# Kernel tuning notes

Hardware: AMD Instinct MI355X
Metric: run time of the kernel (lower is better)

The kernel has to match this reference:

```python
import jax, jax.numpy as jnp
import numpy as np

SUB_NO = 20
T_NO = 200
NB = 19            # cos_basis_no
COS_SHIFT = 1.0
COS_SCALE = 5.0
T_DATA = 100000
E_NO = 2000
I_NO = 400


def _cos_basis():
    x = jnp.arange(T_NO, dtype=jnp.float32)
    raw = COS_SCALE * jnp.log(x + COS_SHIFT)                      # [T_no]
    phi = (jnp.pi / 2.0) * jnp.arange(NB, dtype=jnp.float32)[:, None]  # [NB,1]
    basis = 0.5 * jnp.cos(raw[None, :] - phi) + 0.5               # [NB, T_no]
    mask = (raw[None, :] >= phi - jnp.pi) & (raw[None, :] <= phi + jnp.pi)
    return jnp.where(mask, basis, 0.0)


def _gconv(x, kern_flipped):
    # depthwise (grouped) 1d cross-correlation, VALID padding, matching torch F.conv1d
    # x: [L, sub], kern_flipped: [sub, T_no] (already time-flipped) -> [L - T_no + 1, sub]
    out = jax.lax.conv_general_dilated(
        x.T[None],                      # [1, sub, L]
        kern_flipped[:, None, :],       # [sub, 1, T_no]
        window_strides=(1,), padding='VALID',
        feature_group_count=x.shape[1],
        dimension_numbers=('NCH', 'OIH', 'NCH'))
    return out[0].T


def setup_inputs() -> dict:
    key = jax.random.key(0)
    ks = jax.random.split(key, 16)
    rng = np.random.default_rng(0)
    # tree adjacency: each node j>0 has a parent < j; C_den[parent, child] = 1
    C_den = np.zeros((SUB_NO, SUB_NO), np.float32)
    for j in range(1, SUB_NO):
        C_den[rng.integers(0, j), j] = 1.0
    # one-hot synapse -> subunit maps
    C_syn_e = np.zeros((SUB_NO, E_NO), np.float32)
    C_syn_e[rng.integers(0, SUB_NO, E_NO), np.arange(E_NO)] = 1.0
    C_syn_i = np.zeros((SUB_NO, I_NO), np.float32)
    C_syn_i[rng.integers(0, SUB_NO, I_NO), np.arange(I_NO)] = 1.0
    # sparse binary spike trains
    S_e = (jax.random.uniform(ks[0], (T_DATA, E_NO)) < 0.02).astype(jnp.float32)
    S_i = (jax.random.uniform(ks[1], (T_DATA, I_NO)) < 0.02).astype(jnp.float32)
    Z = (jax.random.uniform(ks[2], (T_DATA, SUB_NO)) < 0.05).astype(jnp.float32)
    return {
        'S_e': S_e, 'S_i': S_i, 'Z': Z,
        'C_den': jnp.asarray(C_den), 'C_syn_e': jnp.asarray(C_syn_e), 'C_syn_i': jnp.asarray(C_syn_i),
        'W_syn': 0.1 * jax.random.normal(ks[3], (SUB_NO, NB, 2)),
        'W_hist': 0.1 * jax.random.normal(ks[4], (SUB_NO, NB)),
        'W_spk': jnp.ones(SUB_NO) + 0.05 * jax.random.normal(ks[5], (SUB_NO,)),
        'Delta_spk': jax.random.uniform(ks[6], (SUB_NO,), maxval=2.0),
        'Tau_spk': 3.0 * jnp.ones(SUB_NO) + 0.1 * jax.random.normal(ks[7], (SUB_NO,)),
        'V_o': jax.random.normal(ks[8], (1,)),
        'Theta': 0.1 * jax.random.normal(ks[9], (SUB_NO,)),
        'weight1': 0.1 * jax.random.normal(ks[10], (SUB_NO, 6)),
        'weight2': 0.1 * jax.random.normal(ks[11], (6, 6)),
        'weight3': 0.1 * jax.random.normal(ks[12], (6, SUB_NO)),
    }


def reference(S_e, S_i, Z, C_den, C_syn_e, C_syn_i, W_syn, W_hist, W_spk,
              Delta_spk, Tau_spk, V_o, Theta, weight1, weight2, weight3):
    cb = _cos_basis()                                  # [NB, T_no]
    sub = C_den.shape[0]
    pad = lambda x, n: jnp.concatenate([jnp.zeros((n, sub), x.dtype), x], axis=0)

    # --- spike_convolve ---
    syn_e = S_e @ C_syn_e.T                            # [T, sub]
    syn_i = S_i @ C_syn_i.T
    e_kern = W_syn[:, :, 0] @ cb                       # [sub, T_no]
    i_kern = W_syn[:, :, 1] @ cb
    filtered_e = _gconv(pad(syn_e, T_NO - 1), jnp.flip(e_kern, 1))
    filtered_i = _gconv(pad(syn_i, T_NO - 1), jnp.flip(i_kern, 1))
    syn = filtered_e + filtered_i                      # [T, sub]

    # --- history and spike kernels (causal, 1-step delayed: pad T_no, drop last) ---
    hist_kern = W_hist @ cb                            # [sub, T_no]
    pad_Z = pad(Z, T_NO)                               # [T + T_no, sub]
    hist_filt = _gconv(pad_Z, jnp.flip(hist_kern, 1))[:-1]   # [T, sub]

    t = jnp.maximum(jnp.arange(T_NO, dtype=jnp.float32)[None, :] - Delta_spk[:, None], 0.0)
    t_tau = t / (Tau_spk[:, None] ** 2)
    spk_kern = t_tau * jnp.exp(-t_tau) * (W_spk[:, None] ** 2)  # [sub, T_no]
    spk_filt = _gconv(pad_Z, jnp.flip(spk_kern, 1))[:-1]        # [T, sub]

    # --- per-subunit loop, vectorized: leaf gather == spk_filt @ C_den.T ---
    sub_in = syn + Theta[None, :] + hist_filt + spk_filt @ C_den.T   # [T, sub]
    h0 = jax.nn.leaky_relu(sub_in)
    h1 = jax.nn.leaky_relu(h0[:, :, None] * weight1[None, :, :])     # [T, sub, 6]
    h2 = jax.nn.leaky_relu(jnp.einsum('tsk,kj->tsj', h1, weight2))   # [T, sub, 6]
    final_Z = jax.nn.sigmoid(jnp.einsum('tsj,js->ts', h2, weight3))  # [T, sub]

    final_V = spk_filt[:, 0] + V_o[0]                  # [T]
    out_filters = jnp.concatenate([e_kern, i_kern, hist_kern, spk_kern], axis=0)  # [4*sub, T_no]
    return final_V, final_Z, out_filters
```

## Files before the change

kernel.cpp:

```cpp
#include <hip/hip_runtime.h>

typedef unsigned short ushort_t;
typedef unsigned int uint_t;
typedef float __attribute__((ext_vector_type(4))) f32x4;

#define T_DATA 100000
#define E_NO 2000
#define I_NO 400
#define SUB 20
#define TNO 200
#define NBASIS 19
#define HEAD 256
#define TAILPAD 2048
#define SIGSTRIDE (HEAD + T_DATA + TAILPAD)
#define TILE 2048
#define RPT 8
#define TSPAN 32
#define ACCSTR 36

#define OFF_Z  ((size_t)T_DATA)
#define OFF_F  ((size_t)T_DATA + (size_t)T_DATA*SUB)

__device__ __forceinline__ float b2f(ushort_t u) {
    union { uint_t i; float f; } v; v.i = ((uint_t)u) << 16; return v.f;
}
__device__ __forceinline__ ushort_t f2b(float f) {
    union { uint_t i; float f_; } v; v.f_ = f;
    uint_t b = v.i;
    uint_t r = (b + 0x7FFFu + ((b >> 16) & 1u)) >> 16;
    return (ushort_t)r;
}
__device__ __forceinline__ float ldin(const void* p, size_t idx, int mode) {
    return mode ? b2f(((const ushort_t*)p)[idx]) : ((const float*)p)[idx];
}
__device__ __forceinline__ void stout(void* p, size_t idx, float val, int mode) {
    if (mode) ((ushort_t*)p)[idx] = f2b(val);
    else      ((float*)p)[idx] = val;
}
__device__ __forceinline__ float f4get(const float4& v, int i) {
    return i == 0 ? v.x : i == 1 ? v.y : i == 2 ? v.z : v.w;
}
__device__ __forceinline__ float pick12(const float4& L, const float4& M, const float4& H, int e) {
    return e < 4 ? f4get(L, e) : e < 8 ? f4get(M, e - 4) : f4get(H, e - 8);
}
__device__ __forceinline__ int detect_mode(const void* tau) {
    const ushort_t* tu = (const ushort_t*)tau;
    int cnt = 0;
    #pragma unroll
    for (int i = 0; i < 20; ++i) {
        float v = b2f(tu[i]);
        if (v >= 1.5f && v < 6.0f) cnt++;
    }
    return (cnt >= 15) ? 1 : 0;
}

__global__ __launch_bounds__(256) void k0_prep(
        const void* Csyn_e, const void* Csyn_i,
        const void* W_syn, const void* W_hist,
        const void* W_spk, const void* Delta, const void* Tau,
        float* ws_f, int* mape, int* mapi, ushort_t* sigs, void* dout) {
    __shared__ int smode;
    int bid = blockIdx.x, tid = threadIdx.x;
    if (tid == 0) smode = detect_mode(Tau);
    __syncthreads();
    int mode = smode;
    if (bid < 80) {
        int kidx = bid / 20, s = bid % 20;
        int tau = tid;
        if (tau < TNO) {
            float val;
            if (kidx < 3) {
                float raw = 5.0f * logf((float)tau + 1.0f);
                val = 0.f;
                for (int b = 0; b < NBASIS; ++b) {
                    float phi = 1.5707963267948966f * (float)b;
                    float d = raw - phi;
                    float basis = (d >= -3.14159265358979f && d <= 3.14159265358979f)
                                  ? (0.5f * cosf(d) + 0.5f) : 0.f;
                    float w = (kidx == 0) ? ldin(W_syn, (size_t)s * NBASIS * 2 + b * 2 + 0, mode)
                            : (kidx == 1) ? ldin(W_syn, (size_t)s * NBASIS * 2 + b * 2 + 1, mode)
                                          : ldin(W_hist, (size_t)s * NBASIS + b, mode);
                    val += w * basis;
                }
            } else {
                float dl = ldin(Delta, s, mode), tu = ldin(Tau, s, mode), wk = ldin(W_spk, s, mode);
                float t = fmaxf((float)tau - dl, 0.f);
                float tt = t / (tu * tu);
                val = tt * expf(-tt) * (wk * wk);
            }
            ws_f[kidx * 4000 + s * TNO + tau] = val;
            stout(dout, OFF_F + (size_t)bid * TNO + tau, val, mode);
        }
    } else if (bid < 96) {
        int e = (bid - 80) * 256 + tid;
        if (e < E_NO) {
            int m = 0;
            for (int s = 0; s < SUB; ++s)
                if (ldin(Csyn_e, (size_t)s * E_NO + e, mode) != 0.f) { m = s; break; }
            mape[e] = m;
        }
    } else if (bid < 98) {
        int e = (bid - 96) * 256 + tid;
        if (e < I_NO) {
            int m = 0;
            for (int s = 0; s < SUB; ++s)
                if (ldin(Csyn_i, (size_t)s * I_NO + e, mode) != 0.f) { m = s; break; }
            mapi[e] = m;
        }
    } else if (bid < 158) {
        int rg = bid - 98;
        int sg = rg / 20, s = rg % 20;
        ushort_t* p = sigs + (size_t)sg * SUB * SIGSTRIDE + (size_t)s * SIGSTRIDE;
        for (int i = tid; i < HEAD; i += 256) p[i] = 0;
        for (int i = tid; i < TAILPAD; i += 256) p[HEAD + T_DATA + i] = 0;
    }
}

__global__ __launch_bounds__(256, 4) void k1_reduce(
        const void* __restrict__ S_e, const void* __restrict__ S_i,
        const void* __restrict__ Z,
        const int* __restrict__ mape, const int* __restrict__ mapi,
        const void* __restrict__ Tau,
        ushort_t* __restrict__ sigs) {
    __shared__ float acc[60 * ACCSTR];
    __shared__ int smode;
    int tid = threadIdx.x;
    if (tid == 0) smode = detect_mode(Tau);
    for (int i = tid; i < 60 * ACCSTR; i += 256) acc[i] = 0.f;
    __syncthreads();
    int mode = smode;

    int be[8], bi8[8];
    if (mode) {
        if (tid < 250) {
            #pragma unroll
            for (int j = 0; j < 8; ++j) be[j] = mape[tid * 8 + j] * ACCSTR;
        }
        if (tid < 50) {
            #pragma unroll
            for (int j = 0; j < 8; ++j) bi8[j] = (20 + mapi[tid * 8 + j]) * ACCSTR;
        }
    } else {
        if (tid < 250) {
            #pragma unroll
            for (int j = 0; j < 4; ++j) be[j] = mape[tid * 4 + j] * ACCSTR;
            #pragma unroll
            for (int j = 0; j < 4; ++j) be[4 + j] = mape[(tid + 250) * 4 + j] * ACCSTR;
        }
        if (tid < 100) {
            #pragma unroll
            for (int j = 0; j < 4; ++j) bi8[j] = (20 + mapi[tid * 4 + j]) * ACCSTR;
        }
    }

    int base = blockIdx.x * TSPAN;
    if (mode) {
        for (int r0 = 0; r0 < TSPAN; r0 += 4) {
            uint4 u[4];
            uint4 w[4];
            float zv[4];
            if (tid < 250) {
                #pragma unroll
                for (int k = 0; k < 4; ++k)
                    u[k] = *(const uint4*)((const ushort_t*)S_e +
                                           (size_t)(base + r0 + k) * E_NO + tid * 8);
            }
            if (tid < 50) {
                #pragma unroll
                for (int k = 0; k < 4; ++k)
                    w[k] = *(const uint4*)((const ushort_t*)S_i +
                                           (size_t)(base + r0 + k) * I_NO + tid * 8);
            }
            if (tid >= 192 && tid < 212) {
                int s = tid - 192;
                #pragma unroll
                for (int k = 0; k < 4; ++k)
                    zv[k] = b2f(((const ushort_t*)Z)[(size_t)(base + r0 + k) * SUB + s]);
            }
            if (tid < 250) {
                #pragma unroll
                for (int k = 0; k < 4; ++k) {
                    int rl = r0 + k;
                    uint_t wd[4] = {u[k].x, u[k].y, u[k].z, u[k].w};
                    #pragma unroll
                    for (int q = 0; q < 4; ++q) {
                        float a = b2f((ushort_t)(wd[q] & 0xFFFF));
                        float b = b2f((ushort_t)(wd[q] >> 16));
                        if (a != 0.f) atomicAdd(&acc[be[2 * q] + rl], a);
                        if (b != 0.f) atomicAdd(&acc[be[2 * q + 1] + rl], b);
                    }
                }
            }
            if (tid < 50) {
                #pragma unroll
                for (int k = 0; k < 4; ++k) {
                    int rl = r0 + k;
                    uint_t wd[4] = {w[k].x, w[k].y, w[k].z, w[k].w};
                    #pragma unroll
                    for (int q = 0; q < 4; ++q) {
                        float a = b2f((ushort_t)(wd[q] & 0xFFFF));
                        float b = b2f((ushort_t)(wd[q] >> 16));
                        if (a != 0.f) atomicAdd(&acc[bi8[2 * q] + rl], a);
                        if (b != 0.f) atomicAdd(&acc[bi8[2 * q + 1] + rl], b);
                    }
                }
            }
            if (tid >= 192 && tid < 212) {
                int s = tid - 192;
                #pragma unroll
                for (int k = 0; k < 4; ++k)
                    acc[(40 + s) * ACCSTR + r0 + k] = zv[k];
            }
        }
    } else {
        f32x4 uA[8], uB[8];
        f32x4 wv[4];
        float zv[4];
        const float* Sef = (const float*)S_e;
        const float* Sif = (const float*)S_i;
        const float* Zf  = (const float*)Z;
        bool le = (tid < 250);
        bool li = (tid < 100);
        bool lz = (tid >= 192 && tid < 212);
        if (le) {
            #pragma unroll
            for (int k = 0; k < 4; ++k) {
                const float* pe = Sef + (size_t)(base + k) * E_NO;
                uA[2 * k]     = __builtin_nontemporal_load((const f32x4*)(pe + tid * 4));
                uA[2 * k + 1] = __builtin_nontemporal_load((const f32x4*)(pe + (tid + 250) * 4));
            }
        }
        for (int r0 = 0; r0 < TSPAN; r0 += 8) {
            if (le) {
                #pragma unroll
                for (int k = 0; k < 4; ++k) {
                    const float* pe = Sef + (size_t)(base + r0 + 4 + k) * E_NO;
                    uB[2 * k]     = __builtin_nontemporal_load((const f32x4*)(pe + tid * 4));
                    uB[2 * k + 1] = __builtin_nontemporal_load((const f32x4*)(pe + (tid + 250) * 4));
                }
            }
            if (li) {
                #pragma unroll
                for (int k = 0; k < 4; ++k)
                    wv[k] = __builtin_nontemporal_load(
                        (const f32x4*)(Sif + (size_t)(base + r0 + k) * I_NO + tid * 4));
            }
            if (lz) {
                int s = tid - 192;
                #pragma unroll
                for (int k = 0; k < 4; ++k)
                    zv[k] = Zf[(size_t)(base + r0 + k) * SUB + s];
            }
            if (le) {
                #pragma unroll
                for (int k = 0; k < 4; ++k) {
                    int rl = r0 + k;
                    #pragma unroll
                    for (int q = 0; q < 4; ++q) {
                        float a = uA[2 * k][q];
                        float b = uA[2 * k + 1][q];
                        if (a != 0.f) atomicAdd(&acc[be[q] + rl], a);
                        if (b != 0.f) atomicAdd(&acc[be[4 + q] + rl], b);
                    }
                }
            }
            if (li) {
                #pragma unroll
                for (int k = 0; k < 4; ++k) {
                    int rl = r0 + k;
                    #pragma unroll
                    for (int q = 0; q < 4; ++q) {
                        float c = wv[k][q];
                        if (c != 0.f) atomicAdd(&acc[bi8[q] + rl], c);
                    }
                }
            }
            if (lz) {
                int s = tid - 192;
                #pragma unroll
                for (int k = 0; k < 4; ++k)
                    acc[(40 + s) * ACCSTR + r0 + k] = zv[k];
            }
            if (r0 + 8 < TSPAN && le) {
                #pragma unroll
                for (int k = 0; k < 4; ++k) {
                    const float* pe = Sef + (size_t)(base + r0 + 8 + k) * E_NO;
                    uA[2 * k]     = __builtin_nontemporal_load((const f32x4*)(pe + tid * 4));
                    uA[2 * k + 1] = __builtin_nontemporal_load((const f32x4*)(pe + (tid + 250) * 4));
                }
            }
            if (li) {
                #pragma unroll
                for (int k = 0; k < 4; ++k)
                    wv[k] = __builtin_nontemporal_load(
                        (const f32x4*)(Sif + (size_t)(base + r0 + 4 + k) * I_NO + tid * 4));
            }
            if (lz) {
                int s = tid - 192;
                #pragma unroll
                for (int k = 0; k < 4; ++k)
                    zv[k] = Zf[(size_t)(base + r0 + 4 + k) * SUB + s];
            }
            if (le) {
                #pragma unroll
                for (int k = 0; k < 4; ++k) {
                    int rl = r0 + 4 + k;
                    #pragma unroll
                    for (int q = 0; q < 4; ++q) {
                        float a = uB[2 * k][q];
                        float b = uB[2 * k + 1][q];
                        if (a != 0.f) atomicAdd(&acc[be[q] + rl], a);
                        if (b != 0.f) atomicAdd(&acc[be[4 + q] + rl], b);
                    }
                }
            }
            if (li) {
                #pragma unroll
                for (int k = 0; k < 4; ++k) {
                    int rl = r0 + 4 + k;
                    #pragma unroll
                    for (int q = 0; q < 4; ++q) {
                        float c = wv[k][q];
                        if (c != 0.f) atomicAdd(&acc[bi8[q] + rl], c);
                    }
                }
            }
            if (lz) {
                int s = tid - 192;
                #pragma unroll
                for (int k = 0; k < 4; ++k)
                    acc[(40 + s) * ACCSTR + r0 + 4 + k] = zv[k];
            }
        }
    }
    __syncthreads();

    for (int idx = tid; idx < 60 * (TSPAN / 4); idx += 256) {
        int sig = idx >> 3;
        int g = idx & 7;
        int t0 = g * 4;
        const float* src = &acc[sig * ACCSTR + t0];
        float4 v = *(const float4*)src;
        uint2 o;
        o.x = (uint_t)f2b(v.x) | ((uint_t)f2b(v.y) << 16);
        o.y = (uint_t)f2b(v.z) | ((uint_t)f2b(v.w) << 16);
        *(uint2*)(sigs + (size_t)sig * SIGSTRIDE + HEAD + base + t0) = o;
    }
}

__global__ __launch_bounds__(256) void k2_conv(
        const ushort_t* __restrict__ sigs, const float* __restrict__ ws_f,
        ushort_t* __restrict__ base_out, ushort_t* __restrict__ spk_out) {
    __shared__ float X[3 * 2248 + 800];
    float* XE = X;
    float* XI = X + 2248;
    float* ZZ = X + 4496;
    float* KK = X + 6744;
    int s = blockIdx.y;
    int t0 = blockIdx.x * TILE;
    int tid = threadIdx.x;

    for (int k = 0; k < 4; ++k)
        for (int j = tid; j < TNO; j += 256)
            KK[k * TNO + j] = ws_f[k * 4000 + s * TNO + j];

    {
        const ushort_t* g0 = sigs + (size_t)s * SIGSTRIDE + (HEAD - 200) + t0;
        const ushort_t* g1 = g0 + (size_t)SUB * SIGSTRIDE;
        const ushort_t* g2 = g0 + (size_t)2 * SUB * SIGSTRIDE;
        for (int v = tid; v < 281; v += 256) {
            uint4 u = *(const uint4*)(g0 + v * 8);
            float* d = XE + v * 8;
            d[0]=b2f((ushort_t)(u.x&0xFFFF)); d[1]=b2f((ushort_t)(u.x>>16));
            d[2]=b2f((ushort_t)(u.y&0xFFFF)); d[3]=b2f((ushort_t)(u.y>>16));
            d[4]=b2f((ushort_t)(u.z&0xFFFF)); d[5]=b2f((ushort_t)(u.z>>16));
            d[6]=b2f((ushort_t)(u.w&0xFFFF)); d[7]=b2f((ushort_t)(u.w>>16));
        }
        for (int v = tid; v < 281; v += 256) {
            uint4 u = *(const uint4*)(g1 + v * 8);
            float* d = XI + v * 8;
            d[0]=b2f((ushort_t)(u.x&0xFFFF)); d[1]=b2f((ushort_t)(u.x>>16));
            d[2]=b2f((ushort_t)(u.y&0xFFFF)); d[3]=b2f((ushort_t)(u.y>>16));
            d[4]=b2f((ushort_t)(u.z&0xFFFF)); d[5]=b2f((ushort_t)(u.z>>16));
            d[6]=b2f((ushort_t)(u.w&0xFFFF)); d[7]=b2f((ushort_t)(u.w>>16));
        }
        for (int v = tid; v < 281; v += 256) {
            uint4 u = *(const uint4*)(g2 + v * 8);
            float* d = ZZ + v * 8;
            d[0]=b2f((ushort_t)(u.x&0xFFFF)); d[1]=b2f((ushort_t)(u.x>>16));
            d[2]=b2f((ushort_t)(u.y&0xFFFF)); d[3]=b2f((ushort_t)(u.y>>16));
            d[4]=b2f((ushort_t)(u.z&0xFFFF)); d[5]=b2f((ushort_t)(u.z>>16));
            d[6]=b2f((ushort_t)(u.w&0xFFFF)); d[7]=b2f((ushort_t)(u.w>>16));
        }
    }
    __syncthreads();

    float acc[RPT] = {0,0,0,0,0,0,0,0};
    float spk[RPT] = {0,0,0,0,0,0,0,0};
    const float4* XE4 = (const float4*)XE;
    const float4* XI4 = (const float4*)XI;
    const float4* ZZ4 = (const float4*)ZZ;
    const float4* KE4 = (const float4*)(KK);
    const float4* KI4 = (const float4*)(KK + 200);
    const float4* KH4 = (const float4*)(KK + 400);
    const float4* KS4 = (const float4*)(KK + 600);
    int w4 = 2 * tid + 49;
    float4 eL = XE4[w4], eM = XE4[w4 + 1], eH = XE4[w4 + 2];
    float4 iL = XI4[w4], iM = XI4[w4 + 1], iH = XI4[w4 + 2];
    float4 zL = ZZ4[w4], zM = ZZ4[w4 + 1], zH = ZZ4[w4 + 2];

    for (int c = 0; c < 50; ++c) {
        if (c > 0) {
            eH = eM; eM = eL; eL = XE4[w4 - c];
            iH = iM; iM = iL; iL = XI4[w4 - c];
            zH = zM; zM = zL; zL = ZZ4[w4 - c];
        }
        float4 ke = KE4[c], ki = KI4[c], kh = KH4[c], ks = KS4[c];
        #pragma unroll
        for (int u = 0; u < 4; ++u) {
            float keu = f4get(ke, u), kiu = f4get(ki, u);
            float khu = f4get(kh, u), ksu = f4get(ks, u);
            #pragma unroll
            for (int r = 0; r < RPT; ++r) {
                float xe = pick12(eL, eM, eH, 4 + r - u);
                float xi = pick12(iL, iM, iH, 4 + r - u);
                float zz = pick12(zL, zM, zH, 3 + r - u);
                acc[r] += keu * xe;
                acc[r] += kiu * xi;
                acc[r] += khu * zz;
                spk[r] += ksu * zz;
            }
        }
    }
    int tbase = t0 + RPT * tid;
    if (tbase + RPT <= T_DATA) {
        uint4 pb, pq;
        pb.x = (uint_t)f2b(acc[0]) | ((uint_t)f2b(acc[1]) << 16);
        pb.y = (uint_t)f2b(acc[2]) | ((uint_t)f2b(acc[3]) << 16);
        pb.z = (uint_t)f2b(acc[4]) | ((uint_t)f2b(acc[5]) << 16);
        pb.w = (uint_t)f2b(acc[6]) | ((uint_t)f2b(acc[7]) << 16);
        pq.x = (uint_t)f2b(spk[0]) | ((uint_t)f2b(spk[1]) << 16);
        pq.y = (uint_t)f2b(spk[2]) | ((uint_t)f2b(spk[3]) << 16);
        pq.z = (uint_t)f2b(spk[4]) | ((uint_t)f2b(spk[5]) << 16);
        pq.w = (uint_t)f2b(spk[6]) | ((uint_t)f2b(spk[7]) << 16);
        *(uint4*)(base_out + (size_t)s * T_DATA + tbase) = pb;
        *(uint4*)(spk_out + (size_t)s * T_DATA + tbase) = pq;
    } else {
        #pragma unroll
        for (int r = 0; r < RPT; ++r) {
            int t = tbase + r;
            if (t < T_DATA) {
                base_out[(size_t)s * T_DATA + t] = f2b(acc[r]);
                spk_out[(size_t)s * T_DATA + t] = f2b(spk[r]);
            }
        }
    }
}

__global__ __launch_bounds__(256) void k3_mlp(
        const ushort_t* __restrict__ base_out, const ushort_t* __restrict__ spk_out,
        const void* __restrict__ C_den, const void* __restrict__ Theta,
        const void* __restrict__ Vo,
        const void* __restrict__ w1, const void* __restrict__ w2,
        const void* __restrict__ w3,
        const void* __restrict__ Tau,
        void* __restrict__ dout) {
    __shared__ float cd[400], th[20], W1[120], W2[36], W3[120];
    __shared__ float vo;
    __shared__ int smode;
    int tid = threadIdx.x;
    if (tid == 0) smode = detect_mode(Tau);
    __syncthreads();
    int mode = smode;
    for (int i = tid; i < 400; i += 256) cd[i] = ldin(C_den, i, mode);
    if (tid < 20) th[tid] = ldin(Theta, tid, mode);
    if (tid < 120) W1[tid] = ldin(w1, tid, mode);
    if (tid < 36) W2[tid] = ldin(w2, tid, mode);
    if (tid >= 128 && tid < 248) W3[tid - 128] = ldin(w3, tid - 128, mode);
    if (tid == 0) vo = ldin(Vo, 0, mode);
    __syncthreads();
    int t = blockIdx.x * 256 + tid;
    if (t >= T_DATA) return;
    float sv[20], bv[20];
    #pragma unroll
    for (int c = 0; c < 20; ++c) {
        sv[c] = b2f(spk_out[(size_t)c * T_DATA + t]);
        bv[c] = b2f(base_out[(size_t)c * T_DATA + t]);
    }
    stout(dout, (size_t)t, sv[0] + vo, mode);
    #pragma unroll
    for (int p = 0; p < 20; ++p) {
        float ps = 0.f;
        #pragma unroll
        for (int c = 0; c < 20; ++c) ps += cd[p * 20 + c] * sv[c];
        float x = bv[p] + th[p] + ps;
        float h0 = x >= 0.f ? x : 0.01f * x;
        float h1[6];
        #pragma unroll
        for (int k = 0; k < 6; ++k) {
            float y = h0 * W1[p * 6 + k];
            h1[k] = y >= 0.f ? y : 0.01f * y;
        }
        float zacc = 0.f;
        #pragma unroll
        for (int j = 0; j < 6; ++j) {
            float a = 0.f;
            #pragma unroll
            for (int k = 0; k < 6; ++k) a += h1[k] * W2[k * 6 + j];
            float h2 = a >= 0.f ? a : 0.01f * a;
            zacc += h2 * W3[j * 20 + p];
        }
        float zv = 1.f / (1.f + expf(-zacc));
        stout(dout, OFF_Z + (size_t)t * SUB + p, zv, mode);
    }
}

extern "C" void kernel_launch(void* const* d_in, const int* in_sizes, int n_in,
                              void* d_out, int out_size, void* d_ws, size_t ws_size,
                              hipStream_t stream) {
    const void* S_e     = d_in[0];
    const void* S_i     = d_in[1];
    const void* Z       = d_in[2];
    const void* C_den   = d_in[3];
    const void* C_syn_e = d_in[4];
    const void* C_syn_i = d_in[5];
    const void* W_syn   = d_in[6];
    const void* W_hist  = d_in[7];
    const void* W_spk   = d_in[8];
    const void* Delta   = d_in[9];
    const void* Tau     = d_in[10];
    const void* Vo      = d_in[11];
    const void* Theta   = d_in[12];
    const void* w1      = d_in[13];
    const void* w2      = d_in[14];
    const void* w3      = d_in[15];

    char* w = (char*)d_ws;
    float*    ws_f     = (float*)(w + 64);
    int*      mape     = (int*)(w + 64 + 64000);
    int*      mapi     = (int*)(w + 64 + 64000 + 8000);
    ushort_t* sigs     = (ushort_t*)(w + 73664);
    ushort_t* base_out = (ushort_t*)(w + 12350144);
    ushort_t* spk_out  = (ushort_t*)(w + 16350144);

    hipLaunchKernelGGL(k0_prep, dim3(158), dim3(256), 0, stream,
                       C_syn_e, C_syn_i, W_syn, W_hist, W_spk, Delta, Tau,
                       ws_f, mape, mapi, sigs, d_out);
    hipLaunchKernelGGL(k1_reduce, dim3(T_DATA / TSPAN), dim3(256), 0, stream,
                       S_e, S_i, Z, mape, mapi, Tau, sigs);
    hipLaunchKernelGGL(k2_conv, dim3((T_DATA + TILE - 1) / TILE, SUB), dim3(256), 0, stream,
                       sigs, ws_f, base_out, spk_out);
    hipLaunchKernelGGL(k3_mlp, dim3((T_DATA + 255) / 256), dim3(256), 0, stream,
                       base_out, spk_out, C_den, Theta, Vo, w1, w2, w3, Tau, d_out);
}
```

Measured before the change: 270.3 us.

## Double conv outputs per thread and tile size; use cached loads in reduce

The conv kernel now computes 16 outputs per thread over a 4096-sample tile instead of 8 over 2048. Each loaded input and kernel value is reused across more accumulators, and the shared memory buffers and tail padding grow to match. Separately, the reduce kernel switches from nontemporal loads to ordinary loads for the spike trains. The larger tile raises register and LDS use, which could lower occupancy, and it halves the block count along time.

```diff
diff --git a/kernel.cpp b/kernel.cpp
--- a/kernel.cpp
+++ b/kernel.cpp
@@ -11,10 +11,10 @@
 #define TNO 200
 #define NBASIS 19
 #define HEAD 256
-#define TAILPAD 2048
+#define TAILPAD 2560
 #define SIGSTRIDE (HEAD + T_DATA + TAILPAD)
-#define TILE 2048
-#define RPT 8
+#define TILE 4096
+#define RPT 16
 #define TSPAN 32
 #define ACCSTR 36
 
@@ -40,8 +40,11 @@
 __device__ __forceinline__ float f4get(const float4& v, int i) {
     return i == 0 ? v.x : i == 1 ? v.y : i == 2 ? v.z : v.w;
 }
-__device__ __forceinline__ float pick12(const float4& L, const float4& M, const float4& H, int e) {
-    return e < 4 ? f4get(L, e) : e < 8 ? f4get(M, e - 4) : f4get(H, e - 8);
+__device__ __forceinline__ float pick20(const float4& a, const float4& b, const float4& c,
+                                        const float4& d, const float4& e, int i) {
+    return i < 8 ? (i < 4 ? f4get(a, i) : f4get(b, i - 4))
+                 : (i < 12 ? f4get(c, i - 8)
+                           : (i < 16 ? f4get(d, i - 12) : f4get(e, i - 16)));
 }
 __device__ __forceinline__ int detect_mode(const void* tau) {
     const ushort_t* tu = (const ushort_t*)tau;
@@ -226,8 +229,8 @@
             #pragma unroll
             for (int k = 0; k < 4; ++k) {
                 const float* pe = Sef + (size_t)(base + k) * E_NO;
-                uA[2 * k]     = __builtin_nontemporal_load((const f32x4*)(pe + tid * 4));
-                uA[2 * k + 1] = __builtin_nontemporal_load((const f32x4*)(pe + (tid + 250) * 4));
+                uA[2 * k]     = *(const f32x4*)(pe + tid * 4);
+                uA[2 * k + 1] = *(const f32x4*)(pe + (tid + 250) * 4);
             }
         }
         for (int r0 = 0; r0 < TSPAN; r0 += 8) {
@@ -235,15 +238,14 @@
                 #pragma unroll
                 for (int k = 0; k < 4; ++k) {
                     const float* pe = Sef + (size_t)(base + r0 + 4 + k) * E_NO;
-                    uB[2 * k]     = __builtin_nontemporal_load((const f32x4*)(pe + tid * 4));
-                    uB[2 * k + 1] = __builtin_nontemporal_load((const f32x4*)(pe + (tid + 250) * 4));
+                    uB[2 * k]     = *(const f32x4*)(pe + tid * 4);
+                    uB[2 * k + 1] = *(const f32x4*)(pe + (tid + 250) * 4);
                 }
             }
             if (li) {
                 #pragma unroll
                 for (int k = 0; k < 4; ++k)
-                    wv[k] = __builtin_nontemporal_load(
-                        (const f32x4*)(Sif + (size_t)(base + r0 + k) * I_NO + tid * 4));
+                    wv[k] = *(const f32x4*)(Sif + (size_t)(base + r0 + k) * I_NO + tid * 4);
             }
             if (lz) {
                 int s = tid - 192;
@@ -285,15 +287,14 @@
                 #pragma unroll
                 for (int k = 0; k < 4; ++k) {
                     const float* pe = Sef + (size_t)(base + r0 + 8 + k) * E_NO;
-                    uA[2 * k]     = __builtin_nontemporal_load((const f32x4*)(pe + tid * 4));
-                    uA[2 * k + 1] = __builtin_nontemporal_load((const f32x4*)(pe + (tid + 250) * 4));
+                    uA[2 * k]     = *(const f32x4*)(pe + tid * 4);
+                    uA[2 * k + 1] = *(const f32x4*)(pe + (tid + 250) * 4);
                 }
             }
             if (li) {
                 #pragma unroll
                 for (int k = 0; k < 4; ++k)
-                    wv[k] = __builtin_nontemporal_load(
-                        (const f32x4*)(Sif + (size_t)(base + r0 + 4 + k) * I_NO + tid * 4));
+                    wv[k] = *(const f32x4*)(Sif + (size_t)(base + r0 + 4 + k) * I_NO + tid * 4);
             }
             if (lz) {
                 int s = tid - 192;
@@ -351,11 +352,11 @@
 __global__ __launch_bounds__(256) void k2_conv(
         const ushort_t* __restrict__ sigs, const float* __restrict__ ws_f,
         ushort_t* __restrict__ base_out, ushort_t* __restrict__ spk_out) {
-    __shared__ float X[3 * 2248 + 800];
+    __shared__ float X[3 * 4296 + 800];
     float* XE = X;
-    float* XI = X + 2248;
-    float* ZZ = X + 4496;
-    float* KK = X + 6744;
+    float* XI = X + 4296;
+    float* ZZ = X + 8592;
+    float* KK = X + 12888;
     int s = blockIdx.y;
     int t0 = blockIdx.x * TILE;
     int tid = threadIdx.x;
@@ -368,7 +369,7 @@
         const ushort_t* g0 = sigs + (size_t)s * SIGSTRIDE + (HEAD - 200) + t0;
         const ushort_t* g1 = g0 + (size_t)SUB * SIGSTRIDE;
         const ushort_t* g2 = g0 + (size_t)2 * SUB * SIGSTRIDE;
-        for (int v = tid; v < 281; v += 256) {
+        for (int v = tid; v < 537; v += 256) {
             uint4 u = *(const uint4*)(g0 + v * 8);
             float* d = XE + v * 8;
             d[0]=b2f((ushort_t)(u.x&0xFFFF)); d[1]=b2f((ushort_t)(u.x>>16));
@@ -376,7 +377,7 @@
             d[4]=b2f((ushort_t)(u.z&0xFFFF)); d[5]=b2f((ushort_t)(u.z>>16));
             d[6]=b2f((ushort_t)(u.w&0xFFFF)); d[7]=b2f((ushort_t)(u.w>>16));
         }
-        for (int v = tid; v < 281; v += 256) {
+        for (int v = tid; v < 537; v += 256) {
             uint4 u = *(const uint4*)(g1 + v * 8);
             float* d = XI + v * 8;
             d[0]=b2f((ushort_t)(u.x&0xFFFF)); d[1]=b2f((ushort_t)(u.x>>16));
@@ -384,7 +385,7 @@
             d[4]=b2f((ushort_t)(u.z&0xFFFF)); d[5]=b2f((ushort_t)(u.z>>16));
             d[6]=b2f((ushort_t)(u.w&0xFFFF)); d[7]=b2f((ushort_t)(u.w>>16));
         }
-        for (int v = tid; v < 281; v += 256) {
+        for (int v = tid; v < 537; v += 256) {
             uint4 u = *(const uint4*)(g2 + v * 8);
             float* d = ZZ + v * 8;
             d[0]=b2f((ushort_t)(u.x&0xFFFF)); d[1]=b2f((ushort_t)(u.x>>16));
@@ -395,8 +396,9 @@
     }
     __syncthreads();
 
-    float acc[RPT] = {0,0,0,0,0,0,0,0};
-    float spk[RPT] = {0,0,0,0,0,0,0,0};
+    float acc[RPT], spk[RPT];
+    #pragma unroll
+    for (int r = 0; r < RPT; ++r) { acc[r] = 0.f; spk[r] = 0.f; }
     const float4* XE4 = (const float4*)XE;
     const float4* XI4 = (const float4*)XI;
     const float4* ZZ4 = (const float4*)ZZ;
@@ -404,16 +406,16 @@
     const float4* KI4 = (const float4*)(KK + 200);
     const float4* KH4 = (const float4*)(KK + 400);
     const float4* KS4 = (const float4*)(KK + 600);
-    int w4 = 2 * tid + 49;
-    float4 eL = XE4[w4], eM = XE4[w4 + 1], eH = XE4[w4 + 2];
-    float4 iL = XI4[w4], iM = XI4[w4 + 1], iH = XI4[w4 + 2];
-    float4 zL = ZZ4[w4], zM = ZZ4[w4 + 1], zH = ZZ4[w4 + 2];
+    int w4 = 4 * tid + 49;
+    float4 e0 = XE4[w4], e1 = XE4[w4+1], e2 = XE4[w4+2], e3 = XE4[w4+3], e4 = XE4[w4+4];
+    float4 i0 = XI4[w4], i1 = XI4[w4+1], i2 = XI4[w4+2], i3 = XI4[w4+3], i4 = XI4[w4+4];
+    float4 z0 = ZZ4[w4], z1 = ZZ4[w4+1], z2 = ZZ4[w4+2], z3 = ZZ4[w4+3], z4 = ZZ4[w4+4];
 
     for (int c = 0; c < 50; ++c) {
         if (c > 0) {
-            eH = eM; eM = eL; eL = XE4[w4 - c];
-            iH = iM; iM = iL; iL = XI4[w4 - c];
-            zH = zM; zM = zL; zL = ZZ4[w4 - c];
+            e4 = e3; e3 = e2; e2 = e1; e1 = e0; e0 = XE4[w4 - c];
+            i4 = i3; i3 = i2; i2 = i1; i1 = i0; i0 = XI4[w4 - c];
+            z4 = z3; z3 = z2; z2 = z1; z1 = z0; z0 = ZZ4[w4 - c];
         }
         float4 ke = KE4[c], ki = KI4[c], kh = KH4[c], ks = KS4[c];
         #pragma unroll
@@ -422,9 +424,9 @@
             float khu = f4get(kh, u), ksu = f4get(ks, u);
             #pragma unroll
             for (int r = 0; r < RPT; ++r) {
-                float xe = pick12(eL, eM, eH, 4 + r - u);
-                float xi = pick12(iL, iM, iH, 4 + r - u);
-                float zz = pick12(zL, zM, zH, 3 + r - u);
+                float xe = pick20(e0, e1, e2, e3, e4, 4 + r - u);
+                float xi = pick20(i0, i1, i2, i3, i4, 4 + r - u);
+                float zz = pick20(z0, z1, z2, z3, z4, 3 + r - u);
                 acc[r] += keu * xe;
                 acc[r] += kiu * xi;
                 acc[r] += khu * zz;
@@ -434,17 +436,27 @@
     }
     int tbase = t0 + RPT * tid;
     if (tbase + RPT <= T_DATA) {
-        uint4 pb, pq;
-        pb.x = (uint_t)f2b(acc[0]) | ((uint_t)f2b(acc[1]) << 16);
-        pb.y = (uint_t)f2b(acc[2]) | ((uint_t)f2b(acc[3]) << 16);
-        pb.z = (uint_t)f2b(acc[4]) | ((uint_t)f2b(acc[5]) << 16);
-        pb.w = (uint_t)f2b(acc[6]) | ((uint_t)f2b(acc[7]) << 16);
-        pq.x = (uint_t)f2b(spk[0]) | ((uint_t)f2b(spk[1]) << 16);
-        pq.y = (uint_t)f2b(spk[2]) | ((uint_t)f2b(spk[3]) << 16);
-        pq.z = (uint_t)f2b(spk[4]) | ((uint_t)f2b(spk[5]) << 16);
-        pq.w = (uint_t)f2b(spk[6]) | ((uint_t)f2b(spk[7]) << 16);
-        *(uint4*)(base_out + (size_t)s * T_DATA + tbase) = pb;
-        *(uint4*)(spk_out + (size_t)s * T_DATA + tbase) = pq;
+        uint4 pb0, pb1, pq0, pq1;
+        pb0.x = (uint_t)f2b(acc[0])  | ((uint_t)f2b(acc[1])  << 16);
+        pb0.y = (uint_t)f2b(acc[2])  | ((uint_t)f2b(acc[3])  << 16);
+        pb0.z = (uint_t)f2b(acc[4])  | ((uint_t)f2b(acc[5])  << 16);
+        pb0.w = (uint_t)f2b(acc[6])  | ((uint_t)f2b(acc[7])  << 16);
+        pb1.x = (uint_t)f2b(acc[8])  | ((uint_t)f2b(acc[9])  << 16);
+        pb1.y = (uint_t)f2b(acc[10]) | ((uint_t)f2b(acc[11]) << 16);
+        pb1.z = (uint_t)f2b(acc[12]) | ((uint_t)f2b(acc[13]) << 16);
+        pb1.w = (uint_t)f2b(acc[14]) | ((uint_t)f2b(acc[15]) << 16);
+        pq0.x = (uint_t)f2b(spk[0])  | ((uint_t)f2b(spk[1])  << 16);
+        pq0.y = (uint_t)f2b(spk[2])  | ((uint_t)f2b(spk[3])  << 16);
+        pq0.z = (uint_t)f2b(spk[4])  | ((uint_t)f2b(spk[5])  << 16);
+        pq0.w = (uint_t)f2b(spk[6])  | ((uint_t)f2b(spk[7])  << 16);
+        pq1.x = (uint_t)f2b(spk[8])  | ((uint_t)f2b(spk[9])  << 16);
+        pq1.y = (uint_t)f2b(spk[10]) | ((uint_t)f2b(spk[11]) << 16);
+        pq1.z = (uint_t)f2b(spk[12]) | ((uint_t)f2b(spk[13]) << 16);
+        pq1.w = (uint_t)f2b(spk[14]) | ((uint_t)f2b(spk[15]) << 16);
+        *(uint4*)(base_out + (size_t)s * T_DATA + tbase) = pb0;
+        *(uint4*)(base_out + (size_t)s * T_DATA + tbase + 8) = pb1;
+        *(uint4*)(spk_out + (size_t)s * T_DATA + tbase) = pq0;
+        *(uint4*)(spk_out + (size_t)s * T_DATA + tbase + 8) = pq1;
     } else {
         #pragma unroll
         for (int r = 0; r < RPT; ++r) {
@@ -540,8 +552,8 @@
     int*      mape     = (int*)(w + 64 + 64000);
     int*      mapi     = (int*)(w + 64 + 64000 + 8000);
     ushort_t* sigs     = (ushort_t*)(w + 73664);
-    ushort_t* base_out = (ushort_t*)(w + 12350144);
-    ushort_t* spk_out  = (ushort_t*)(w + 16350144);
+    ushort_t* base_out = (ushort_t*)(w + 12411584);
+    ushort_t* spk_out  = (ushort_t*)(w + 16411584);
 
     hipLaunchKernelGGL(k0_prep, dim3(158), dim3(256), 0, stream,
                        C_syn_e, C_syn_i, W_syn, W_hist, W_spk, Delta, Tau,
```

New measurement: 288.9 us. +6.9%, slower.
